# Performance work log

Measured on AMD Instinct MI355X. Metric: run time of the kernel, lower is better.

Reference implementation:

```python
import jax, jax.numpy as jnp
import numpy as np

N_HEAD, N_KV_HEAD, HEAD_DIM = 16, 4, 128
EPS = 1e-5


def rms_norm(x, eps=EPS):
    return x * jax.lax.rsqrt(jnp.mean(x * x, axis=-1, keepdims=True) + eps)


def apply_rope(x, cos, sin):
    # x: (B,T,H,D); cos/sin: (1,T,1,D//2)
    d = x.shape[-1] // 2
    x1, x2 = x[..., :d], x[..., d:]
    return jnp.concatenate([x1 * cos - x2 * sin, x1 * sin + x2 * cos], axis=-1)


def setup_inputs() -> dict:
    key = jax.random.key(0)
    ks = jax.random.split(key, 6)
    B, T, C = 4, 2048, 2048
    H, KV, D = N_HEAD, N_KV_HEAD, HEAD_DIM
    x = jax.random.normal(ks[0], (B, T, C), dtype=jnp.float32)
    # RoPE tables (llama-style, theta=10000)
    inv_freq = 1.0 / (10000.0 ** (jnp.arange(D // 2, dtype=jnp.float32) / (D // 2)))
    ang = jnp.arange(T, dtype=jnp.float32)[:, None] * inv_freq[None, :]  # (T, D/2)
    cos = jnp.cos(ang)[None, :, None, :]
    sin = jnp.sin(ang)[None, :, None, :]
    s = 0.02
    wq = jax.random.normal(ks[1], (C, H * D), dtype=jnp.float32) * s
    wk = jax.random.normal(ks[2], (C, KV * D), dtype=jnp.float32) * s
    wv = jax.random.normal(ks[3], (C, KV * D), dtype=jnp.float32) * s
    wproj = jax.random.normal(ks[4], (H * D, C), dtype=jnp.float32) * s
    return {"x": x, "cos": cos, "sin": sin, "wq": wq, "wk": wk, "wv": wv, "wproj": wproj}


def reference(x, cos, sin, wq, wk, wv, wproj):
    B, T, C = x.shape
    H, KV, D = N_HEAD, N_KV_HEAD, HEAD_DIM
    n_rep = H // KV
    q = (x @ wq).reshape(B, T, H, D)
    k = (x @ wk).reshape(B, T, KV, D)
    v = (x @ wv).reshape(B, T, KV, D)
    q = apply_rope(q, cos, sin)
    k = apply_rope(k, cos, sin)
    # QK-norm (use_qk_norm=True)
    q = rms_norm(q)
    k = rms_norm(k)
    # GQA: expand kv heads (matches torch repeat_interleave on head dim)
    k = jnp.repeat(k, n_rep, axis=2)
    v = jnp.repeat(v, n_rep, axis=2)
    scale = 1.0 / np.sqrt(D).astype(np.float32)
    scores = jnp.einsum('bqhd,bkhd->bhqk', q, k) * scale  # (B,H,T,T)
    causal = jnp.tril(jnp.ones((T, T), dtype=bool))
    scores = jnp.where(causal[None, None], scores, jnp.finfo(scores.dtype).min)
    p = jax.nn.softmax(scores, axis=-1)
    y = jnp.einsum('bhqk,bkhd->bqhd', p, v).reshape(B, T, H * D)
    return y @ wproj
```

## Files before the change

### kernel.cpp

```cpp
#include <hip/hip_runtime.h>
#include <hip/hip_bf16.h>
#include <stdint.h>

using bf16 = __hip_bfloat16;
typedef __attribute__((ext_vector_type(8))) short short8;
typedef __attribute__((ext_vector_type(4))) float f32x4;
typedef __attribute__((ext_vector_type(16))) float f32x16;

#define MFMA16(a,b,c) __builtin_amdgcn_mfma_f32_16x16x32_bf16(a,b,c,0,0,0)
#define MFMA32(a,b,c) __builtin_amdgcn_mfma_f32_32x32x16_bf16(a,b,c,0,0,0)

__device__ __forceinline__ void gload_lds16(const void* g, void* l) {
  __builtin_amdgcn_global_load_lds((const __attribute__((address_space(1))) void*)g,
                                   (__attribute__((address_space(3))) void*)l, 16, 0, 0);
}

__device__ __forceinline__ short bf_bits(float f) {
  bf16 h = __float2bfloat16(f);
  return *reinterpret_cast<short*>(&h);
}
__device__ __forceinline__ unsigned int pk2(float a, float b) {
  return ((unsigned int)(unsigned short)bf_bits(b) << 16) | (unsigned short)bf_bits(a);
}
__device__ __forceinline__ float bf2f(short s) {
  return __uint_as_float((unsigned int)(unsigned short)s << 16);
}

__global__ __launch_bounds__(256) void f32_to_bf16_k(const float* __restrict__ in,
                                                     bf16* __restrict__ out, size_t n) {
  size_t i = ((size_t)blockIdx.x * 256 + threadIdx.x) * 8;
  if (i >= n) return;
  float4 a = *(const float4*)(in + i);
  float4 b = *(const float4*)(in + i + 4);
  short8 pk;
  pk[0] = bf_bits(a.x); pk[1] = bf_bits(a.y); pk[2] = bf_bits(a.z); pk[3] = bf_bits(a.w);
  pk[4] = bf_bits(b.x); pk[5] = bf_bits(b.y); pk[6] = bf_bits(b.z); pk[7] = bf_bits(b.w);
  *(short8*)(out + i) = pk;
}

__global__ __launch_bounds__(256) void transpose_cvt_k(const float* __restrict__ in,
                                                       bf16* __restrict__ out, int K, int N) {
  __shared__ float tile[32][33];
  int n0 = blockIdx.x * 32, k0 = blockIdx.y * 32;
  int tx = threadIdx.x & 31, ty = threadIdx.x >> 5;
#pragma unroll
  for (int j = 0; j < 4; ++j) {
    int kk = ty + j * 8;
    tile[kk][tx] = in[(size_t)(k0 + kk) * N + n0 + tx];
  }
  __syncthreads();
#pragma unroll
  for (int j = 0; j < 4; ++j) {
    int nn = ty + j * 8;
    out[(size_t)(n0 + nn) * K + k0 + tx] = __float2bfloat16(tile[tx][nn]);
  }
}

__global__ __launch_bounds__(256) void transpose_v_k(const bf16* __restrict__ qkv,
                                                     bf16* __restrict__ vt) {
  constexpr int T = 2048, Dh = 128, KV = 4, QKVW = 3072, VOFF = 2560;
  __shared__ bf16 tile[32][33];
  int t0 = blockIdx.x * 32, d0 = blockIdx.y * 32;
  int b = blockIdx.z >> 2, kv = blockIdx.z & 3;
  int tx = threadIdx.x & 31, ty = threadIdx.x >> 5;
#pragma unroll
  for (int j = 0; j < 4; ++j) {
    int tt = ty + j * 8;
    tile[tt][tx] = qkv[((size_t)(b * T + t0 + tt)) * QKVW + VOFF + kv * Dh + d0 + tx];
  }
  __syncthreads();
#pragma unroll
  for (int j = 0; j < 4; ++j) {
    int dd = ty + j * 8;
    vt[((size_t)((b * KV + kv) * Dh + d0 + dd)) * T + t0 + tx] = tile[tx][dd];
  }
}

__global__ __launch_bounds__(256) void rope_rms_k(bf16* __restrict__ buf, int rowstride,
                                                  int baseoff,
                                                  const float* __restrict__ cosp,
                                                  const float* __restrict__ sinp,
                                                  int nh, float outscale) {
  constexpr int T = 2048;
  int wid = blockIdx.x * 4 + (threadIdx.x >> 6);
  int lane = threadIdx.x & 63;
  int h = wid % nh;
  int tok = wid / nh;
  int t = tok & (T - 1);
  bf16* p = buf + (size_t)tok * rowstride + baseoff + h * 128;
  float x1 = __bfloat162float(p[lane]);
  float x2 = __bfloat162float(p[lane + 64]);
  float c = cosp[t * 64 + lane], s = sinp[t * 64 + lane];
  float o1 = x1 * c - x2 * s;
  float o2 = x1 * s + x2 * c;
  float ss = o1 * o1 + o2 * o2;
#pragma unroll
  for (int m = 1; m < 64; m <<= 1) ss += __shfl_xor(ss, m, 64);
  float r = rsqrtf(ss * (1.f / 128.f) + 1e-5f) * outscale;
  p[lane] = __float2bfloat16(o1 * r);
  p[lane + 64] = __float2bfloat16(o2 * r);
}

#define PHASE(buf, i0, ...)                                                       \
  {                                                                               \
    short8 a00 = ldA(buf, i0, 0), a01 = ldA(buf, i0, 1);                          \
    short8 a10 = ldA(buf, (i0) + 1, 0), a11 = ldA(buf, (i0) + 1, 1);              \
    __VA_ARGS__;                                                                  \
    __builtin_amdgcn_s_barrier();                                                 \
    asm volatile("s_waitcnt lgkmcnt(0)" ::: "memory");                            \
    __builtin_amdgcn_s_setprio(1);                                                \
    _Pragma("unroll") for (int j = 0; j < 4; ++j) {                               \
      acc[i0][j] = MFMA16(a00, bf_[2 * j], acc[i0][j]);                           \
      acc[i0][j] = MFMA16(a01, bf_[2 * j + 1], acc[i0][j]);                       \
      acc[(i0) + 1][j] = MFMA16(a10, bf_[2 * j], acc[(i0) + 1][j]);               \
      acc[(i0) + 1][j] = MFMA16(a11, bf_[2 * j + 1], acc[(i0) + 1][j]);           \
    }                                                                             \
    __builtin_amdgcn_s_setprio(0);                                                \
  }
#define LOADB(buf)                                                                \
  _Pragma("unroll") for (int j = 0; j < 4; ++j) {                                 \
    bf_[2 * j] = ldB(buf, j, 0);                                                  \
    bf_[2 * j + 1] = ldB(buf, j, 1);                                              \
  }
#define BAR __builtin_amdgcn_s_barrier()

template <typename OutT>
__global__ __launch_bounds__(512, 2) void gemm256(const bf16* __restrict__ A,
                                                  const bf16* __restrict__ Bt,
                                                  OutT* __restrict__ C, int K,
                                                  int NT, int ldC) {
  __shared__ char lds[131072];
  const int tid = threadIdx.x, lane = tid & 63, w = tid >> 6;
  const int wm = w >> 2, wn = w & 3;
  const int bx = blockIdx.x;
  const int chunk = gridDim.x >> 3;
  const int wgid = (bx & 7) * chunk + (bx >> 3);
  const int m0 = (wgid / NT) * 256, n0 = (wgid % NT) * 256;
  const int lm = lane & 15;
  const int sw = (lane & 7) << 4;
  const int g16 = (lane >> 4) << 4;
  const size_t strideAB = (size_t)K * 2;

  auto stageA = [&](int buf, int h, int t) {
#pragma unroll
    for (int p2 = 0; p2 < 2; ++p2) {
      int off = tid * 16 + p2 * 8192;
      int row = off >> 7, cb = off & 127;
      int scb = cb ^ ((row & 7) << 4);
      gload_lds16((const char*)A + (size_t)(m0 + h * 128 + row) * strideAB + t * 128 + scb,
                  lds + buf * 65536 + h * 16384 + off);
    }
  };
  auto stageB = [&](int buf, int h, int t) {
#pragma unroll
    for (int p2 = 0; p2 < 2; ++p2) {
      int off = tid * 16 + p2 * 8192;
      int row = off >> 7, cb = off & 127;
      int scb = cb ^ ((row & 7) << 4);
      gload_lds16((const char*)Bt + (size_t)(n0 + h * 128 + row) * strideAB + t * 128 + scb,
                  lds + buf * 65536 + 32768 + h * 16384 + off);
    }
  };
  auto ldA = [&](int buf, int i, int ks) {
    int row = wm * 128 + i * 16 + lm;
    return *(const short8*)(lds + buf * 65536 + row * 128 + ((ks * 64 + g16) ^ sw));
  };
  auto ldB = [&](int buf, int j, int ks) {
    int row = wn * 64 + j * 16 + lm;
    return *(const short8*)(lds + buf * 65536 + 32768 + row * 128 + ((ks * 64 + g16) ^ sw));
  };

  f32x4 acc[8][4] = {};
  short8 bf_[8];
  const int niter = K / 128;

  stageA(0, 0, 0); stageA(0, 1, 0); stageB(0, 0, 0); stageB(0, 1, 0);
  stageB(1, 0, 1); stageB(1, 1, 1);
  asm volatile("s_waitcnt vmcnt(4)" ::: "memory");
  BAR;

  for (int i = 0; i < niter; ++i) {
    const int t0 = 2 * i, t1 = 2 * i + 1;
    const bool nl = (i + 1 < niter);
    LOADB(0);
    PHASE(0, 0, stageA(1, 0, t1)); BAR;
    PHASE(0, 2, stageA(1, 1, t1)); BAR;
    PHASE(0, 4, if (nl) stageB(0, 0, t0 + 2)); BAR;
    PHASE(0, 6, if (nl) stageB(0, 1, t0 + 2));
    if (nl) { asm volatile("s_waitcnt vmcnt(4)" ::: "memory"); }
    else    { asm volatile("s_waitcnt vmcnt(0)" ::: "memory"); }
    BAR;
    LOADB(1);
    PHASE(1, 0, if (nl) stageA(0, 0, t0 + 2)); BAR;
    PHASE(1, 2, if (nl) stageA(0, 1, t0 + 2)); BAR;
    PHASE(1, 4, if (nl) stageB(1, 0, t1 + 2)); BAR;
    PHASE(1, 6, if (nl) stageB(1, 1, t1 + 2));
    if (nl) { asm volatile("s_waitcnt vmcnt(4)" ::: "memory"); }
    BAR;
  }

  if constexpr (sizeof(OutT) == 2) {
    __syncthreads();
    bf16* sC = (bf16*)lds;
#pragma unroll
    for (int i = 0; i < 8; ++i) {
      int row = wm * 128 + i * 16 + (lane >> 4) * 4;
#pragma unroll
      for (int j = 0; j < 4; ++j) {
        int col = wn * 64 + j * 16 + lm;
#pragma unroll
        for (int r = 0; r < 4; ++r) sC[(row + r) * 256 + col] = __float2bfloat16(acc[i][j][r]);
      }
    }
    __syncthreads();
#pragma unroll
    for (int p = 0; p < 16; ++p) {
      int off = tid * 16 + p * 8192;
      int row = off >> 9, cb = off & 511;
      *(short8*)((char*)C + ((size_t)(m0 + row) * ldC + n0) * 2 + cb) =
          *(const short8*)(lds + off);
    }
  } else {
#pragma unroll
    for (int i = 0; i < 8; ++i) {
      int row = m0 + wm * 128 + i * 16 + (lane >> 4) * 4;
#pragma unroll
      for (int j = 0; j < 4; ++j) {
        int col = n0 + wn * 64 + j * 16 + lm;
#pragma unroll
        for (int r = 0; r < 4; ++r) C[(size_t)(row + r) * ldC + col] = acc[i][j][r];
      }
    }
  }
}

template <typename OutT>
__global__ __launch_bounds__(256) void gemm_bt(const bf16* __restrict__ A,
                                               const bf16* __restrict__ Bt,
                                               OutT* __restrict__ C, int K,
                                               int NT, int ldC) {
  constexpr int BM = 128, BN = 128, BK = 64;
  __shared__ char smem[32768];
  bf16* sA = (bf16*)smem;
  bf16* sB = (bf16*)(smem + 16384);
  int tid = threadIdx.x;
  int lane = tid & 63, w = tid >> 6;
  int flat = blockIdx.x;
  int wgid = (flat & 7) * (gridDim.x >> 3) + (flat >> 3);
  int m0 = (wgid / NT) * BM, n0 = (wgid % NT) * BN;
  int wm = (w >> 1) * 64, wn = (w & 1) * 64;
  f32x4 acc[4][4] = {};
  int nk = K / BK;
  for (int kt = 0; kt < nk; ++kt) {
    __syncthreads();
    int kb = kt * BK;
#pragma unroll
    for (int it = 0; it < 4; ++it) {
      int off = tid * 16 + it * 4096;
      int row = off >> 7, cb = off & 127;
      gload_lds16((const char*)A + (((size_t)(m0 + row)) * K + kb) * 2 + cb, (char*)sA + off);
    }
#pragma unroll
    for (int it = 0; it < 4; ++it) {
      int off = tid * 16 + it * 4096;
      int row = off >> 7, cb = off & 127;
      gload_lds16((const char*)Bt + (((size_t)(n0 + row)) * K + kb) * 2 + cb, (char*)sB + off);
    }
    asm volatile("s_waitcnt vmcnt(0)" ::: "memory");
    __syncthreads();
#pragma unroll
    for (int ks = 0; ks < 2; ++ks) {
      short8 af[4], bfr[4];
#pragma unroll
      for (int i = 0; i < 4; ++i) {
        af[i]  = *(const short8*)(sA + (wm + i * 16 + (lane & 15)) * BK + ks * 32 + (lane >> 4) * 8);
        bfr[i] = *(const short8*)(sB + (wn + i * 16 + (lane & 15)) * BK + ks * 32 + (lane >> 4) * 8);
      }
#pragma unroll
      for (int i = 0; i < 4; ++i)
#pragma unroll
        for (int j = 0; j < 4; ++j)
          acc[i][j] = MFMA16(af[i], bfr[j], acc[i][j]);
    }
  }
  if constexpr (sizeof(OutT) == 2) {
    __syncthreads();
    bf16* sC = (bf16*)smem;
#pragma unroll
    for (int i = 0; i < 4; ++i) {
      int row = wm + i * 16 + (lane >> 4) * 4;
#pragma unroll
      for (int j = 0; j < 4; ++j) {
        int col = wn + j * 16 + (lane & 15);
#pragma unroll
        for (int r = 0; r < 4; ++r)
          sC[(row + r) * BN + col] = __float2bfloat16(acc[i][j][r]);
      }
    }
    __syncthreads();
#pragma unroll
    for (int it = 0; it < 8; ++it) {
      int off = tid * 16 + it * 4096;
      int row = off >> 8, cb = off & 255;
      *(short8*)((char*)C + ((size_t)(m0 + row) * ldC + n0) * 2 + cb) =
          *(const short8*)(smem + off);
    }
  } else {
#pragma unroll
    for (int i = 0; i < 4; ++i) {
      int row = m0 + wm + i * 16 + (lane >> 4) * 4;
#pragma unroll
      for (int j = 0; j < 4; ++j) {
        int col = n0 + wn + j * 16 + (lane & 15);
#pragma unroll
        for (int r = 0; r < 4; ++r)
          C[(size_t)(row + r) * ldC + col] = acc[i][j][r];
      }
    }
  }
}

__global__ __launch_bounds__(512, 2) void attn_k(const bf16* __restrict__ qkv,
                                                 const bf16* __restrict__ vt,
                                                 bf16* __restrict__ y,
                                                 const float* __restrict__ cosp,
                                                 const float* __restrict__ sinp) {
  constexpr int T = 2048, Dh = 128, KV = 4, KB = 64, QKVW = 3072, KOFF = 2048;
  __shared__ char lds[65536];
  const int tid = threadIdx.x, lane = tid & 63, w = tid >> 6;
  const int hi = lane >> 5, lq = lane & 31;
  const int bx = blockIdx.x;
  const int qt = 7 - (bx >> 6);
  const int b = (bx >> 4) & 3, h = bx & 15;
  const int kh = h >> 2;
  const int q0 = qt * 256 + w * 32;
  const int qg = q0 + lq;
  const int swz = (lane & 7) << 4;

  short8 aq[8];
  {
    const bf16* qp = qkv + ((size_t)(b * T + qg)) * QKVW + h * Dh + hi * 8;
#pragma unroll
    for (int m = 0; m < 8; ++m) aq[m] = *(const short8*)(qp + m * 16);
  }
  __builtin_amdgcn_s_waitcnt(0);

  {
    float ss = 0.f;
#pragma unroll
    for (int m = 0; m < 8; ++m)
#pragma unroll
      for (int e = 0; e < 8; ++e) { float v = bf2f(aq[m][e]); ss += v * v; }
    ss += __shfl_xor(ss, 32, 64);
    float rn = rsqrtf(ss * (1.f / 128.f) + 1e-5f) * 0.08838834764831845f;
    const float4* cq4 = (const float4*)(cosp + (size_t)qg * 64) + hi * 2;
    const float4* sq4 = (const float4*)(sinp + (size_t)qg * 64) + hi * 2;
#pragma unroll
    for (int m = 0; m < 4; ++m) {
      float4 c0 = cq4[m * 4], c1 = cq4[m * 4 + 1];
      float4 s0 = sq4[m * 4], s1 = sq4[m * 4 + 1];
      float cc[8] = {c0.x, c0.y, c0.z, c0.w, c1.x, c1.y, c1.z, c1.w};
      float sn[8] = {s0.x, s0.y, s0.z, s0.w, s1.x, s1.y, s1.z, s1.w};
      short8 xl = aq[m], xh = aq[m + 4], nl, nh;
#pragma unroll
      for (int e = 0; e < 8; ++e) {
        float x1 = bf2f(xl[e]), x2 = bf2f(xh[e]);
        nl[e] = bf_bits((x1 * cc[e] - x2 * sn[e]) * rn);
        nh[e] = bf_bits((x1 * sn[e] + x2 * cc[e]) * rn);
      }
      aq[m] = nl; aq[m + 4] = nh;
    }
  }

  f32x16 acc[4] = {};
  float mrow = -1e4f, lrow = 0.f;

  auto stage = [&](int buf, int kv0) {
#pragma unroll
    for (int p = 0; p < 2; ++p) {
      int off = tid * 16 + p * 8192;
      int row = off >> 8, cb = off & 255;
      int scb = cb ^ ((row & 7) << 4);
      gload_lds16((const char*)qkv + (((size_t)(b * T + kv0 + row)) * QKVW + KOFF + kh * Dh) * 2 + scb,
                  lds + buf * 16384 + off);
    }
#pragma unroll
    for (int p = 0; p < 2; ++p) {
      int off = tid * 16 + p * 8192;
      int row = off >> 7, cb = off & 127;
      int scb = cb ^ ((row & 7) << 4);
      gload_lds16((const char*)vt + (((size_t)((b * KV + kh) * Dh + row)) * T + kv0) * 2 + scb,
                  lds + 32768 + buf * 16384 + off);
    }
  };

  const int nt = (qt + 1) * 4;
  const int lastit = (q0 + 31) >> 6;
  stage(0, 0);

  for (int it = 0; it < nt; ++it) {
    int cur = it & 1;
    if (it + 1 < nt) { stage(cur ^ 1, (it + 1) * KB); asm volatile("s_waitcnt vmcnt(4)" ::: "memory"); }
    else             { asm volatile("s_waitcnt vmcnt(0)" ::: "memory"); }
    __builtin_amdgcn_s_barrier();
    if (it <= lastit) {
      const char* sK = lds + cur * 16384;
      const char* sV = lds + 32768 + cur * 16384;
      const int kv0 = it * KB;

      f32x16 s0 = {}, s1 = {};
      __builtin_amdgcn_s_setprio(1);
#pragma unroll
      for (int m = 0; m < 8; ++m) {
        short8 ak = *(const short8*)(sK + lq * 256 + ((m * 32 + hi * 16) ^ swz));
        s0 = MFMA32(ak, aq[m], s0);
      }
#pragma unroll
      for (int m = 0; m < 8; ++m) {
        short8 ak = *(const short8*)(sK + (32 + lq) * 256 + ((m * 32 + hi * 16) ^ swz));
        s1 = MFMA32(ak, aq[m], s1);
      }
      __builtin_amdgcn_s_setprio(0);

      if (kv0 + 63 > q0) {
#pragma unroll
        for (int r = 0; r < 16; ++r) {
          int krow = (r & 3) + 8 * (r >> 2) + 4 * hi;
          if (kv0 + krow > qg) s0[r] = -1e30f;
          if (kv0 + 32 + krow > qg) s1[r] = -1e30f;
        }
      }

      float tmax = s0[0];
#pragma unroll
      for (int r = 1; r < 16; ++r) tmax = fmaxf(tmax, s0[r]);
#pragma unroll
      for (int r = 0; r < 16; ++r) tmax = fmaxf(tmax, s1[r]);
      tmax = fmaxf(tmax, __shfl_xor(tmax, 32, 64));
      if (!__all(tmax - mrow <= 8.0f)) {
        float mn = fmaxf(mrow, tmax);
        float corr = __expf(mrow - mn);
        mrow = mn;
        lrow *= corr;
#pragma unroll
        for (int dt = 0; dt < 4; ++dt)
#pragma unroll
          for (int r = 0; r < 16; ++r) acc[dt][r] *= corr;
      }
      float rsum = 0.f;
#pragma unroll
      for (int r = 0; r < 16; ++r) { s0[r] = __expf(s0[r] - mrow); rsum += s0[r]; }
#pragma unroll
      for (int r = 0; r < 16; ++r) { s1[r] = __expf(s1[r] - mrow); rsum += s1[r]; }
      rsum += __shfl_xor(rsum, 32, 64);
      lrow += rsum;

      unsigned int u[16];
#pragma unroll
      for (int g = 0; g < 4; ++g) {
        u[g * 2 + 0] = pk2(s0[4 * g + 0], s0[4 * g + 1]);
        u[g * 2 + 1] = pk2(s0[4 * g + 2], s0[4 * g + 3]);
        u[8 + g * 2 + 0] = pk2(s1[4 * g + 0], s1[4 * g + 1]);
        u[8 + g * 2 + 1] = pk2(s1[4 * g + 2], s1[4 * g + 3]);
      }
      short8 pb[4];
#pragma unroll
      for (int kvs = 0; kvs < 4; ++kvs) {
        unsigned int lo0 = u[4 * kvs + 0], lo1 = u[4 * kvs + 1];
        unsigned int hi0 = u[4 * kvs + 2], hi1 = u[4 * kvs + 3];
        asm volatile("v_permlane32_swap_b32 %0, %1" : "+v"(lo0), "+v"(hi0));
        asm volatile("v_permlane32_swap_b32 %0, %1" : "+v"(lo1), "+v"(hi1));
        union { short8 v; unsigned int q[4]; } P;
        P.q[0] = lo0; P.q[1] = lo1; P.q[2] = hi0; P.q[3] = hi1;
        pb[kvs] = P.v;
      }

      __builtin_amdgcn_s_setprio(1);
#pragma unroll
      for (int dt = 0; dt < 4; ++dt) {
#pragma unroll
        for (int kvs = 0; kvs < 4; ++kvs) {
          short8 av = *(const short8*)(sV + (dt * 32 + lq) * 128 + ((kvs * 32 + hi * 16) ^ swz));
          acc[dt] = MFMA32(av, pb[kvs], acc[dt]);
        }
      }
      __builtin_amdgcn_s_setprio(0);
    }
    __builtin_amdgcn_s_barrier();
  }

  float inv = 1.f / lrow;
  __syncthreads();
  char* myO = lds + w * 8192;
#pragma unroll
  for (int dt = 0; dt < 4; ++dt)
#pragma unroll
    for (int i = 0; i < 8; ++i) {
      int d = ((2 * i) & 3) + 8 * (i >> 1) + 4 * hi;
      unsigned int pkd = pk2(acc[dt][2 * i] * inv, acc[dt][2 * i + 1] * inv);
      *(unsigned int*)(myO + lq * 256 + ((dt * 64 + d * 2) ^ ((lq & 7) << 4))) = pkd;
    }
  __syncthreads();
  const int row0 = b * T + qt * 256;
#pragma unroll
  for (int p = 0; p < 8; ++p) {
    int off = (p * 512 + tid) * 16;
    int q = off >> 8, cb = off & 255;
    short8 v = *(const short8*)(lds + (q >> 5) * 8192 + (q & 31) * 256 + (cb ^ ((q & 7) << 4)));
    *(short8*)((char*)y + ((size_t)(row0 + q) * 2048 + h * 128) * 2 + cb) = v;
  }
}

extern "C" void kernel_launch(void* const* d_in, const int* in_sizes, int n_in,
                              void* d_out, int out_size, void* d_ws, size_t ws_size,
                              hipStream_t stream) {
  const float* x    = (const float*)d_in[0];
  const float* cosp = (const float*)d_in[1];
  const float* sinp = (const float*)d_in[2];
  const float* wq   = (const float*)d_in[3];
  const float* wk   = (const float*)d_in[4];
  const float* wv   = (const float*)d_in[5];
  const float* wp   = (const float*)d_in[6];
  float* out = (float*)d_out;

  constexpr size_t Mtok = 8192;
  constexpr int Cdim = 2048, HD = 2048, KVD = 512, QKVW = 3072;

  char* ws = (char*)d_ws;
  bf16* xb    = (bf16*)ws; ws += Mtok * Cdim * 2;
  bf16* wqkvT = (bf16*)ws; ws += (size_t)QKVW * Cdim * 2;
  bf16* wpT   = (bf16*)ws; ws += (size_t)Cdim * HD * 2;
  bf16* qkv   = (bf16*)ws; ws += Mtok * QKVW * 2;
  bf16* vtb   = (bf16*)ws; ws += Mtok * KVD * 2;
  bf16* yb    = (bf16*)ws; ws += Mtok * HD * 2;

  f32_to_bf16_k<<<dim3(Mtok * Cdim / 8 / 256), 256, 0, stream>>>(x, xb, Mtok * Cdim);
  transpose_cvt_k<<<dim3(HD / 32, Cdim / 32), 256, 0, stream>>>(wq, wqkvT, Cdim, HD);
  transpose_cvt_k<<<dim3(KVD / 32, Cdim / 32), 256, 0, stream>>>(wk, wqkvT + (size_t)2048 * Cdim, Cdim, KVD);
  transpose_cvt_k<<<dim3(KVD / 32, Cdim / 32), 256, 0, stream>>>(wv, wqkvT + (size_t)2560 * Cdim, Cdim, KVD);
  transpose_cvt_k<<<dim3(Cdim / 32, HD / 32), 256, 0, stream>>>(wp, wpT, HD, Cdim);

  gemm256<bf16><<<dim3(256), 512, 0, stream>>>(xb, wqkvT, qkv, Cdim, 8, QKVW);
  gemm_bt<bf16><<<dim3(512), 256, 0, stream>>>(xb, wqkvT + (size_t)2048 * Cdim,
                                               (bf16*)qkv + 2048, Cdim, 8, QKVW);

  rope_rms_k<<<dim3(Mtok * 4 / 4), 256, 0, stream>>>(qkv, QKVW, 2048, cosp, sinp, 4, 1.0f);
  transpose_v_k<<<dim3(64, 4, 16), 256, 0, stream>>>(qkv, vtb);

  attn_k<<<dim3(512), 512, 0, stream>>>(qkv, vtb, yb, cosp, sinp);

  gemm256<float><<<dim3(256), 512, 0, stream>>>(yb, wpT, out, Cdim, 8, 2048);
}
```

Baseline: 322.6 us.

## Use exp2 softmax with folded log2e, tree reductions, packed bf16 cvt, balanced tile order

Folds log2(e) into the query scaling so the softmax can use the hardware exp2 instruction directly instead of __expf. The row max and sum reductions become tree reductions to shorten dependency chains, and the lazy-rescale threshold is adjusted for base 2. P packing now uses the single v_cvt_pk_bf16_f32 instruction. Block-to-q-tile mapping is changed so the first half of blocks goes heavy-to-light and the second half light-to-heavy, aiming to balance causal work across CUs.

```diff
diff --git a/kernel.cpp b/kernel.cpp
--- a/kernel.cpp
+++ b/kernel.cpp
@@ -20,11 +20,14 @@
   return *reinterpret_cast<short*>(&h);
 }
 __device__ __forceinline__ unsigned int pk2(float a, float b) {
-  return ((unsigned int)(unsigned short)bf_bits(b) << 16) | (unsigned short)bf_bits(a);
+  unsigned int r;
+  asm("v_cvt_pk_bf16_f32 %0, %1, %2" : "=v"(r) : "v"(a), "v"(b));
+  return r;
 }
 __device__ __forceinline__ float bf2f(short s) {
   return __uint_as_float((unsigned int)(unsigned short)s << 16);
 }
+__device__ __forceinline__ float exp2g(float x) { return __builtin_amdgcn_exp2f(x); }
 
 __global__ __launch_bounds__(256) void f32_to_bf16_k(const float* __restrict__ in,
                                                      bf16* __restrict__ out, size_t n) {
@@ -330,7 +333,8 @@
   const int tid = threadIdx.x, lane = tid & 63, w = tid >> 6;
   const int hi = lane >> 5, lq = lane & 31;
   const int bx = blockIdx.x;
-  const int qt = 7 - (bx >> 6);
+  const int idx = (bx >> 6) & 3;
+  const int qt = (bx < 256) ? (7 - idx) : idx;
   const int b = (bx >> 4) & 3, h = bx & 15;
   const int kh = h >> 2;
   const int q0 = qt * 256 + w * 32;
@@ -352,7 +356,7 @@
 #pragma unroll
       for (int e = 0; e < 8; ++e) { float v = bf2f(aq[m][e]); ss += v * v; }
     ss += __shfl_xor(ss, 32, 64);
-    float rn = rsqrtf(ss * (1.f / 128.f) + 1e-5f) * 0.08838834764831845f;
+    float rn = rsqrtf(ss * (1.f / 128.f) + 1e-5f) * (0.08838834764831845f * 1.4426950408889634f);
     const float4* cq4 = (const float4*)(cosp + (size_t)qg * 64) + hi * 2;
     const float4* sq4 = (const float4*)(sinp + (size_t)qg * 64) + hi * 2;
 #pragma unroll
@@ -431,15 +435,17 @@
         }
       }
 
-      float tmax = s0[0];
-#pragma unroll
-      for (int r = 1; r < 16; ++r) tmax = fmaxf(tmax, s0[r]);
-#pragma unroll
-      for (int r = 0; r < 16; ++r) tmax = fmaxf(tmax, s1[r]);
-      tmax = fmaxf(tmax, __shfl_xor(tmax, 32, 64));
-      if (!__all(tmax - mrow <= 8.0f)) {
+      float mx[16];
+#pragma unroll
+      for (int r = 0; r < 16; ++r) mx[r] = fmaxf(s0[r], s1[r]);
+#pragma unroll
+      for (int st = 8; st > 0; st >>= 1)
+#pragma unroll
+        for (int r = 0; r < 16; ++r) if (r < st) mx[r] = fmaxf(mx[r], mx[r + st]);
+      float tmax = fmaxf(mx[0], __shfl_xor(mx[0], 32, 64));
+      if (!__all(tmax - mrow <= 11.5f)) {
         float mn = fmaxf(mrow, tmax);
-        float corr = __expf(mrow - mn);
+        float corr = exp2g(mrow - mn);
         mrow = mn;
         lrow *= corr;
 #pragma unroll
@@ -447,13 +453,18 @@
 #pragma unroll
           for (int r = 0; r < 16; ++r) acc[dt][r] *= corr;
       }
-      float rsum = 0.f;
-#pragma unroll
-      for (int r = 0; r < 16; ++r) { s0[r] = __expf(s0[r] - mrow); rsum += s0[r]; }
-#pragma unroll
-      for (int r = 0; r < 16; ++r) { s1[r] = __expf(s1[r] - mrow); rsum += s1[r]; }
-      rsum += __shfl_xor(rsum, 32, 64);
-      lrow += rsum;
+      float sm[16];
+#pragma unroll
+      for (int r = 0; r < 16; ++r) {
+        s0[r] = exp2g(s0[r] - mrow);
+        s1[r] = exp2g(s1[r] - mrow);
+        sm[r] = s0[r] + s1[r];
+      }
+#pragma unroll
+      for (int st = 8; st > 0; st >>= 1)
+#pragma unroll
+        for (int r = 0; r < 16; ++r) if (r < st) sm[r] += sm[r + st];
+      lrow += sm[0] + __shfl_xor(sm[0], 32, 64);
 
       unsigned int u[16];
 #pragma unroll
```

Result: slower. 333.7 us (+3.4%).
